# Kernel tuning notes

Measured on AMD Instinct MI355X. Metric: run time of the kernel, lower is better.

## Reference

```python
import jax, jax.numpy as jnp
import numpy as np

B, S, P, C = 128, 672, 168, 500  # batch, seq_len, pred_len, channels

def setup_inputs() -> dict:
    key = jax.random.key(0)
    k1, k2, k3 = jax.random.split(key, 3)
    x = jax.random.normal(k1, (B, S, C), dtype=jnp.float32)
    # per-channel Linear(seq_len -> pred_len): W[c] is [pred_len, seq_len], b[c] is [pred_len]
    W = jax.random.normal(k2, (C, P, S), dtype=jnp.float32) * (1.0 / np.sqrt(S))
    b = jax.random.normal(k3, (C, P), dtype=jnp.float32) * (1.0 / np.sqrt(S))
    return {"x": x, "W": W, "b": b}

def reference(x, W, b):
    # NLinear: subtract last time step, per-channel linear over time, add back
    seq_last = x[:, -1:, :]                     # [B, 1, C]
    xc = x - seq_last                           # [B, S, C]
    # batched over channels: out[b,p,c] = sum_s xc[b,s,c] * W[c,p,s] + b[c,p]
    out = jnp.einsum('bsc,cps->bpc', xc, W) + b.T[None, :, :]
    return out + seq_last
```

## Files before the change

kernel.cpp:

```cpp
#include <hip/hip_runtime.h>


typedef __attribute__((ext_vector_type(8))) short short8;
typedef __attribute__((ext_vector_type(4))) float floatx4;

namespace {
constexpr int Bn = 128, Sn = 672, Pn = 168, Cn = 500;
constexpr int XQ = Bn * Sn;
constexpr int TC = 64, TS = 96, TROW = TS + 12;
constexpr int NS  = Sn / 32;
constexpr int NPT = 11;
constexpr int WROW = 680;
}

__device__ __forceinline__ unsigned short f2bf(float f) {
  unsigned int u = __builtin_bit_cast(unsigned int, f);
  u += 0x7fffu + ((u >> 16) & 1u);
  return (unsigned short)(u >> 16);
}

__global__ __launch_bounds__(256)
void xpose_kernel(const float* __restrict__ x, unsigned short* __restrict__ xq) {
  __shared__ unsigned short T[TC][TROW];
  const int b  = blockIdx.x;
  const int s0 = blockIdx.y * TS;
  const int c0 = blockIdx.z * TC;
  const int t  = threadIdx.x;

  #pragma unroll
  for (int i = 0; i < 6; ++i) {
    const int idx = t + i * 256;
    const int sr  = idx >> 4;
    const int cq  = (idx & 15) * 4;
    int c = c0 + cq;
    if (c > Cn - 4) c = Cn - 4;
    const int rel = c - c0;
    const float4 xv = *(const float4*)&x[(size_t)(b * Sn + s0 + sr) * Cn + c];
    const float4 xl = *(const float4*)&x[(size_t)(b * Sn + (Sn - 1)) * Cn + c];
    T[rel + 0][sr] = f2bf(xv.x - xl.x);
    T[rel + 1][sr] = f2bf(xv.y - xl.y);
    T[rel + 2][sr] = f2bf(xv.z - xl.z);
    T[rel + 3][sr] = f2bf(xv.w - xl.w);
  }
  __syncthreads();
  #pragma unroll
  for (int i = 0; i < 6; ++i) {
    const int idx = t + i * 256;
    const int cr  = idx / 24;
    const int sq  = (idx % 24) * 4;
    const int c   = c0 + cr;
    if (c >= Cn) continue;
    const ushort4 v = *(const ushort4*)&T[cr][sq];
    *(ushort4*)&xq[(size_t)c * XQ + b * Sn + s0 + sq] = v;
  }
}

#define BAR_LGKM() asm volatile("s_waitcnt lgkmcnt(0)\n\ts_barrier" ::: "memory")

__global__ __launch_bounds__(512, 2)
void gemm_kernel(const unsigned short* __restrict__ xq, const float* __restrict__ W,
                 const float* __restrict__ bias, const float* __restrict__ x,
                 float* __restrict__ out) {
  __shared__ unsigned short Wl[2][16 * WROW];
  __shared__ float xl_l[Bn];
  __shared__ float bi_l[Pn];

  const int bid = blockIdx.x;
  const int xcd = bid & 7, sub = bid >> 3;
  const int c0  = xcd * 62 + (xcd < 4 ? xcd : 4) + sub;

  const int tid  = threadIdx.x;
  const int lane = tid & 63;
  const int wv   = tid >> 6;
  const int r16  = lane & 15;
  const int kg   = lane >> 4;

  int wrow[6], wcol[6];
  #pragma unroll
  for (int k = 0; k < 6; ++k) {
    const int f = tid + 512 * k;
    wrow[k] = f / 168;
    wcol[k] = f % 168;
  }
  const bool w5 = tid < 128;

  float4 w0[6], w1[6];

  auto loadW0 = [&](int pt) {
    #pragma unroll
    for (int k = 0; k < 6; ++k) {
      if (k == 5 && !w5) continue;
      int row = pt * 16 + wrow[k];
      if (row > Pn - 1) row = Pn - 1;
      w0[k] = *(const float4*)&W[((size_t)c0 * Pn + row) * Sn + wcol[k] * 4];
    }
  };
  auto loadW1 = [&](int pt) {
    #pragma unroll
    for (int k = 0; k < 6; ++k) {
      if (k == 5 && !w5) continue;
      int row = pt * 16 + wrow[k];
      if (row > Pn - 1) row = Pn - 1;
      w1[k] = *(const float4*)&W[((size_t)c0 * Pn + row) * Sn + wcol[k] * 4];
    }
  };
  auto writeW0 = [&](int buf) {
    #pragma unroll
    for (int k = 0; k < 6; ++k) {
      if (k == 5 && !w5) continue;
      ushort4 u;
      u.x = f2bf(w0[k].x); u.y = f2bf(w0[k].y);
      u.z = f2bf(w0[k].z); u.w = f2bf(w0[k].w);
      *(ushort4*)&Wl[buf][wrow[k] * WROW + wcol[k] * 4] = u;
    }
  };
  auto writeW1 = [&](int buf) {
    #pragma unroll
    for (int k = 0; k < 6; ++k) {
      if (k == 5 && !w5) continue;
      ushort4 u;
      u.x = f2bf(w1[k].x); u.y = f2bf(w1[k].y);
      u.z = f2bf(w1[k].z); u.w = f2bf(w1[k].w);
      *(ushort4*)&Wl[buf][wrow[k] * WROW + wcol[k] * 4] = u;
    }
  };

  const unsigned short* aBase = xq + (size_t)c0 * XQ + (wv * 16 + r16) * Sn + kg * 8;
  short8 aR[NS];
  auto tile = [&](int pt, int buf) {
    floatx4 acc = (floatx4){0.f, 0.f, 0.f, 0.f};
    const int rdb = r16 * WROW + kg * 8;
    #pragma unroll
    for (int s = 0; s < NS; ++s) {
      const short8 wf = *(const short8*)&Wl[buf][rdb + s * 32];
      acc = __builtin_amdgcn_mfma_f32_16x16x32_bf16(aR[s], wf, acc, 0, 0, 0);
    }
    const int p = pt * 16 + r16;
    if (p < Pn) {
      const float bi = bi_l[p];
      #pragma unroll
      for (int r = 0; r < 4; ++r) {
        const int b = wv * 16 + kg * 4 + r;
        out[((size_t)b * Pn + p) * Cn + c0] = acc[r] + bi + xl_l[b];
      }
    }
  };

  loadW0(0);
  loadW1(1);
  if (tid < Bn) xl_l[tid] = x[((size_t)tid * Sn + (Sn - 1)) * Cn + c0];
  else if (tid < Bn + Pn) bi_l[tid - Bn] = bias[(size_t)c0 * Pn + (tid - Bn)];
  #pragma unroll
  for (int s = 0; s < NS; ++s) aR[s] = *(const short8*)(aBase + s * 32);
  writeW0(0);
  BAR_LGKM();

  #pragma unroll 1
  for (int jj = 0; jj < NPT - 1; jj += 2) {
    writeW1(1);
    loadW0(jj + 2);
    tile(jj, 0);
    BAR_LGKM();
    writeW0(0);
    if (jj + 3 < NPT) loadW1(jj + 3);
    tile(jj + 1, 1);
    BAR_LGKM();
  }
  tile(NPT - 1, 0);
}

extern "C" void kernel_launch(void* const* d_in, const int* in_sizes, int n_in,
                              void* d_out, int out_size, void* d_ws, size_t ws_size,
                              hipStream_t stream) {
  (void)in_sizes; (void)n_in; (void)out_size; (void)ws_size;
  const float* x  = (const float*)d_in[0];
  const float* W  = (const float*)d_in[1];
  const float* bv = (const float*)d_in[2];
  float* out = (float*)d_out;
  unsigned short* xq = (unsigned short*)d_ws;

  hipLaunchKernelGGL(xpose_kernel, dim3(Bn, Sn / TS, (Cn + TC - 1) / TC), dim3(256), 0, stream,
                     x, xq);
  hipLaunchKernelGGL(gemm_kernel, dim3(Cn), dim3(512), 0, stream,
                     xq, W, bv, x, out);
}
```

Baseline: 150.9 us.

## Stage GEMM output channel-major in workspace and transpose with a separate kernel

The GEMM kernel, when the workspace is large enough, now writes its results channel-major into a workspace buffer, where consecutive lanes write contiguous p. A new tiled transpose kernel then moves that buffer through shared memory into the [B,P,C] output with float4 coalesced stores. The goal is to replace the strided single-float output stores (stride of Cn floats) with coalesced writes. The cost is an extra full pass that writes and reads about 43 MB of intermediate data, plus one more kernel launch. If the workspace is too small, it falls back to the original direct-store path.

After: 155.9 us. 3.3% more time.

```diff
diff --git a/kernel.cpp b/kernel.cpp
--- a/kernel.cpp
+++ b/kernel.cpp
@@ -7,10 +7,13 @@
 namespace {
 constexpr int Bn = 128, Sn = 672, Pn = 168, Cn = 500;
 constexpr int XQ = Bn * Sn;
+constexpr int BP = Bn * Pn;
 constexpr int TC = 64, TS = 96, TROW = TS + 12;
 constexpr int NS  = Sn / 32;
 constexpr int NPT = 11;
 constexpr int WROW = 680;
+constexpr size_t XQ_BYTES = (size_t)Cn * XQ * 2;
+constexpr size_t WS_NEED  = XQ_BYTES + (size_t)Cn * BP * 4;
 }
 
 __device__ __forceinline__ unsigned short f2bf(float f) {
@@ -57,10 +60,11 @@
 
 #define BAR_LGKM() asm volatile("s_waitcnt lgkmcnt(0)\n\ts_barrier" ::: "memory")
 
+template <bool TO_WS>
 __global__ __launch_bounds__(512, 2)
 void gemm_kernel(const unsigned short* __restrict__ xq, const float* __restrict__ W,
                  const float* __restrict__ bias, const float* __restrict__ x,
-                 float* __restrict__ out) {
+                 float* __restrict__ out, float* __restrict__ ot) {
   __shared__ unsigned short Wl[2][16 * WROW];
   __shared__ float xl_l[Bn];
   __shared__ float bi_l[Pn];
@@ -141,7 +145,9 @@
       #pragma unroll
       for (int r = 0; r < 4; ++r) {
         const int b = wv * 16 + kg * 4 + r;
-        out[((size_t)b * Pn + p) * Cn + c0] = acc[r] + bi + xl_l[b];
+        const float v = acc[r] + bi + xl_l[b];
+        if (TO_WS) ot[(size_t)c0 * BP + b * Pn + p] = v;
+        else       out[((size_t)b * Pn + p) * Cn + c0] = v;
       }
     }
   };
@@ -169,18 +175,60 @@
   tile(NPT - 1, 0);
 }
 
+__global__ __launch_bounds__(256)
+void otrans_kernel(const float* __restrict__ ot, float* __restrict__ out) {
+  __shared__ float T[64][69];
+  const int bp0 = blockIdx.x * 64;
+  const int c0  = blockIdx.y * 64;
+  const int t   = threadIdx.x;
+  const int rr  = t >> 4;
+  const int qq  = t & 15;
+
+  #pragma unroll
+  for (int i = 0; i < 4; ++i) {
+    const int cr = rr + i * 16;
+    if (c0 + cr < Cn) {
+      const float4 v = *(const float4*)&ot[(size_t)(c0 + cr) * BP + bp0 + qq * 4];
+      T[cr][qq * 4 + 0] = v.x;
+      T[cr][qq * 4 + 1] = v.y;
+      T[cr][qq * 4 + 2] = v.z;
+      T[cr][qq * 4 + 3] = v.w;
+    }
+  }
+  __syncthreads();
+  #pragma unroll
+  for (int i = 0; i < 4; ++i) {
+    const int br = rr + i * 16;
+    const int cq = qq * 4;
+    if (c0 + cq + 3 < Cn) {
+      float4 v;
+      v.x = T[cq + 0][br]; v.y = T[cq + 1][br];
+      v.z = T[cq + 2][br]; v.w = T[cq + 3][br];
+      *(float4*)&out[(size_t)(bp0 + br) * Cn + c0 + cq] = v;
+    }
+  }
+}
+
 extern "C" void kernel_launch(void* const* d_in, const int* in_sizes, int n_in,
                               void* d_out, int out_size, void* d_ws, size_t ws_size,
                               hipStream_t stream) {
-  (void)in_sizes; (void)n_in; (void)out_size; (void)ws_size;
+  (void)in_sizes; (void)n_in; (void)out_size;
   const float* x  = (const float*)d_in[0];
   const float* W  = (const float*)d_in[1];
   const float* bv = (const float*)d_in[2];
   float* out = (float*)d_out;
   unsigned short* xq = (unsigned short*)d_ws;
+  float* ot = (float*)((char*)d_ws + XQ_BYTES);
 
   hipLaunchKernelGGL(xpose_kernel, dim3(Bn, Sn / TS, (Cn + TC - 1) / TC), dim3(256), 0, stream,
                      x, xq);
-  hipLaunchKernelGGL(gemm_kernel, dim3(Cn), dim3(512), 0, stream,
-                     xq, W, bv, x, out);
-}
+  if (ws_size >= WS_NEED) {
+    hipLaunchKernelGGL(gemm_kernel<true>, dim3(Cn), dim3(512), 0, stream,
+                       xq, W, bv, x, out, ot);
+    hipLaunchKernelGGL(otrans_kernel, dim3(BP / 64, (Cn + 63) / 64), dim3(256), 0, stream,
+                       ot, out);
+  } else {
+    hipLaunchKernelGGL(gemm_kernel<false>, dim3(Cn), dim3(512), 0, stream,
+                       xq, W, bv, x, out, ot);
+  }
+}
```
